# Optimization experiments

Hardware: AMD Instinct MI355X
Metric: run time of the kernel (lower is better)

Reference implementation:

```python
import jax, jax.numpy as jnp
import numpy as np

NCE_T = 0.07  # opt.nce_T
EPS = 1e-8    # torch CosineSimilarity eps

def setup_inputs() -> dict:
    key = jax.random.key(0)
    k1, k2, k3 = jax.random.split(key, 3)
    num_patches, C = 4096, 256
    features = jax.random.normal(k1, (2, num_patches, C), dtype=jnp.float32)
    labels_seg = jax.random.randint(k2, (1, 1, 128, 128, 128), 0, 5, dtype=jnp.int32)
    labels_coords = jax.random.randint(k3, (num_patches, 3), 0, 64, dtype=jnp.int32)
    return {"features": features, "labels_seg": labels_seg,
            "labels_coords": labels_coords, "cr_w": 64, "cr_h": 64, "cr_d": 64}

def _sup_nce_loss(features, lab):
    # features: (ntps, N, C); lab: (N,) int class per patch
    ntps, N, C = features.shape
    M = ntps * N
    f = features.reshape(M, C)
    nrm = jnp.linalg.norm(f, axis=-1)  # (M,)
    # cosine similarity = (f @ f^T) / max(|x||y|, eps), then / temperature
    sim = (f @ f.T) / jnp.maximum(nrm[:, None] * nrm[None, :], EPS)
    logits = sim / NCE_T
    logits = logits - jax.lax.stop_gradient(jnp.max(logits, axis=1, keepdims=True))
    pos = (lab[:, None] == lab[None, :]).astype(f.dtype)        # (N,N)
    pos = jnp.tile(pos, (ntps, ntps))                            # (M,M)
    diag_off = 1.0 - jnp.eye(M, dtype=f.dtype)                   # logits_mask
    pos = pos * diag_off
    denom = jnp.log((jnp.exp(logits) * diag_off).sum(1, keepdims=True))
    log_prob = logits - denom
    mean_log_prob_pos = (pos * log_prob).sum(1) / pos.sum(1)
    return -(mean_log_prob_pos.reshape(ntps, N)).mean()

def reference(features, labels_seg, labels_coords, cr_w, cr_h, cr_d):
    # nearest-neighbor downsample of labels to coords_range (torch 'nearest': floor(i*in/out))
    H, W, D = labels_seg.shape[2], labels_seg.shape[3], labels_seg.shape[4]
    iw = (jnp.arange(cr_w) * H) // cr_w
    ih = (jnp.arange(cr_h) * W) // cr_h
    idd = (jnp.arange(cr_d) * D) // cr_d
    seg = labels_seg[0, 0][iw][:, ih][:, :, idd]  # (cr_w, cr_h, cr_d)
    lab = seg[labels_coords[:, 0], labels_coords[:, 1], labels_coords[:, 2]]  # (N,)
    return _sup_nce_loss(features, lab)
```

## Files before the change

kernel.cpp:

```cpp
#include <hip/hip_runtime.h>
#include <hip/hip_bf16.h>

typedef __attribute__((ext_vector_type(4))) float floatx4;

#define C_DIM 256
#define K2_SCALE 20.60992915f
#define LN2F 0.6931471805599453f

__device__ __forceinline__ unsigned int pack4fp8(float a, float b, float c, float d) {
    int w = __builtin_amdgcn_cvt_pk_fp8_f32(a, b, 0, false);
    w = __builtin_amdgcn_cvt_pk_fp8_f32(c, d, w, true);
    return (unsigned int)w;
}

template <int CTRL>
__device__ __forceinline__ float dppadd(float x) {
    int y = __builtin_amdgcn_update_dpp(0, __builtin_bit_cast(int, x),
                                        CTRL, 0xf, 0xf, true);
    return x + __builtin_bit_cast(float, y);
}
__device__ __forceinline__ float row16_sum(float x) {
    x = dppadd<0xB1>(x);
    x = dppadd<0x4E>(x);
    x = dppadd<0x124>(x);
    x = dppadd<0x128>(x);
    return x;
}

__global__ void norm_kernel(const float* __restrict__ f,
                            unsigned char* __restrict__ g2,
                            const int* __restrict__ seg,
                            const int* __restrict__ coords,
                            const int* __restrict__ crw,
                            const int* __restrict__ crh,
                            const int* __restrict__ crd,
                            int* __restrict__ lab,
                            float* __restrict__ acc_done,
                            int N, int H, int W, int D) {
    __shared__ float nrm[16][264];
    const int tid = threadIdx.x;
    const int bid = blockIdx.x;
    const int gid = bid * 256 + tid;
    const int lane = tid & 63;
    const int wave = tid >> 6;

    if (gid == 0) {
        acc_done[0] = 0.0f;
        ((int*)acc_done)[1] = 0;
    }
    if (gid < N) {
        int c0 = coords[3 * gid + 0];
        int c1 = coords[3 * gid + 1];
        int c2 = coords[3 * gid + 2];
        int i0 = (c0 * H) / crw[0];
        int i1 = (c1 * W) / crh[0];
        int i2 = (c2 * D) / crd[0];
        lab[gid] = seg[(i0 * W + i1) * D + i2];
    }

    const int rbase = bid * 16;
#pragma unroll
    for (int q = 0; q < 4; ++q) {
        const int rl = wave * 4 + q;
        const float4 v = ((const float4*)(f + (size_t)(rbase + rl) * C_DIM))[lane];
        float ss = v.x * v.x + v.y * v.y + v.z * v.z + v.w * v.w;
#pragma unroll
        for (int off = 32; off; off >>= 1) ss += __shfl_xor(ss, off, 64);
        const float inv = 1.0f / sqrtf(ss);
        *(float4*)&nrm[rl][lane * 4] = float4{v.x * inv, v.y * inv, v.z * inv, v.w * inv};
    }
    __syncthreads();

    const int k0 = (tid >> 5) * 32 + ((tid >> 3) & 3) * 8;
    const float* ra = &nrm[(2 * tid) & 15][k0];
    const float* rb = &nrm[(2 * tid + 1) & 15][k0];
    uint4 o;
    o.x = pack4fp8(ra[0], ra[1], ra[2], ra[3]);
    o.y = pack4fp8(ra[4], ra[5], ra[6], ra[7]);
    o.z = pack4fp8(rb[0], rb[1], rb[2], rb[3]);
    o.w = pack4fp8(rb[4], rb[5], rb[6], rb[7]);
    *(uint4*)(g2 + (size_t)bid * 4096 + (size_t)tid * 16) = o;
}

__global__ __launch_bounds__(256, 2) void
gram_kernel(const unsigned char* __restrict__ G2,
            const int* __restrict__ lab,
            float* __restrict__ part,
            int M, int labmask, int nt) {
    __shared__ unsigned char Abuf[32768];
    __shared__ unsigned char Bbuf[32768];
    __shared__ float red[2][2][128][3];

    const int tid = threadIdx.x;
    const int bid = blockIdx.x;
    const int lane = tid & 63;
    const int wave = tid >> 6;
    const int waveM = wave >> 1;
    const int waveN = wave & 1;
    const int cc = lane & 15;
    const int cq = lane >> 4;

    const int start = bid * 4 + (bid < 32 ? bid : 32);
    const int len = 4 + (bid < 32 ? 1 : 0);
    int tmPrev = -1;

    for (int s = 0; s < len; ++s) {
        const int idx = start + s;
        float fnt = (float)nt;
        float disc = (2.0f * fnt + 1.0f) * (2.0f * fnt + 1.0f) - 8.0f * (float)idx;
        int tm = (int)((2.0f * fnt + 1.0f - sqrtf(disc)) * 0.5f);
        if (tm < 0) tm = 0;
        if (tm > nt - 1) tm = nt - 1;
        while (tm > 0 && idx < tm * nt - tm * (tm - 1) / 2) --tm;
        while (idx >= (tm + 1) * nt - (tm + 1) * tm / 2) ++tm;
        const int tn = tm + (idx - (tm * nt - tm * (tm - 1) / 2));

        const int rowA0 = tm * 128;
        const int rowB0 = tn * 128;
        const bool diagTile = (tm == tn);

        if (tm != tmPrev) {
            const unsigned char* gA = G2 + (size_t)tm * 32768;
#pragma unroll
            for (int i = 0; i < 8; ++i) {
                const int u = i * 256 + tid;
                __builtin_amdgcn_global_load_lds(
                    (const __attribute__((address_space(1))) void*)(gA + (size_t)u * 16),
                    (__attribute__((address_space(3))) void*)(&Abuf[(u & ~63) * 16]),
                    16, 0, 0);
            }
            tmPrev = tm;
        }
        if (!diagTile) {
            const unsigned char* gB = G2 + (size_t)tn * 32768;
#pragma unroll
            for (int i = 0; i < 8; ++i) {
                const int u = i * 256 + tid;
                __builtin_amdgcn_global_load_lds(
                    (const __attribute__((address_space(1))) void*)(gB + (size_t)u * 16),
                    (__attribute__((address_space(3))) void*)(&Bbuf[(u & ~63) * 16]),
                    16, 0, 0);
            }
        }
        __syncthreads();

        const unsigned char* A = Abuf;
        const unsigned char* B = diagTile ? Abuf : Bbuf;

        floatx4 acc[4][4];
#pragma unroll
        for (int mi = 0; mi < 4; ++mi)
#pragma unroll
            for (int ni = 0; ni < 4; ++ni)
                acc[mi][ni] = floatx4{-1.0f, -1.0f, -1.0f, -1.0f};

#pragma unroll
        for (int ks = 0; ks < 8; ++ks) {
            long af[4], bf[4];
#pragma unroll
            for (int mi = 0; mi < 4; ++mi)
                af[mi] = *(const long*)&A[(size_t)((waveM * 4 + mi) * 8 + ks) * 512 + lane * 8];
#pragma unroll
            for (int ni = 0; ni < 4; ++ni)
                bf[ni] = *(const long*)&B[(size_t)((waveN * 4 + ni) * 8 + ks) * 512 + lane * 8];
#pragma unroll
            for (int mi = 0; mi < 4; ++mi)
#pragma unroll
                for (int ni = 0; ni < 4; ++ni)
                    acc[mi][ni] = __builtin_amdgcn_mfma_f32_16x16x32_fp8_fp8(
                        af[mi], bf[ni], acc[mi][ni], 0, 0, 0);
        }

        int col_lab[4];
#pragma unroll
        for (int ni = 0; ni < 4; ++ni)
            col_lab[ni] = lab[(rowB0 + waveN * 64 + ni * 16 + cc) & labmask];

        float bse[4] = {}, bnu[4] = {}, bct[4] = {};

#pragma unroll
        for (int mi = 0; mi < 4; ++mi) {
#pragma unroll
            for (int r = 0; r < 4; ++r) {
                const int lrow = waveM * 64 + mi * 16 + cq * 4 + r;
                const int grow = rowA0 + lrow;
                const int rl = lab[grow & labmask];
                float se = 0.0f, nu = 0.0f, ct = 0.0f;
#pragma unroll
                for (int ni = 0; ni < 4; ++ni) {
                    const int gcol = rowB0 + waveN * 64 + ni * 16 + cc;
                    const float ls2 = acc[mi][ni][r] * K2_SCALE;
                    const bool valid = (gcol != grow);
                    const float e = valid ? exp2f(ls2) : 0.0f;
                    const bool pos = valid && (col_lab[ni] == rl);
                    const float nuv = pos ? ls2 : 0.0f;
                    const float p = pos ? 1.0f : 0.0f;
                    se += e; nu += nuv; ct += p;
                    bse[ni] += e; bnu[ni] += nuv; bct[ni] += p;
                }
                se = row16_sum(se);
                nu = row16_sum(nu);
                ct = row16_sum(ct);
                if (cc == 0) {
                    red[0][waveN][lrow][0] = se;
                    red[0][waveN][lrow][1] = nu;
                    red[0][waveN][lrow][2] = ct;
                }
            }
        }

        if (!diagTile) {
#pragma unroll
            for (int ni = 0; ni < 4; ++ni) {
                float se = bse[ni], nu = bnu[ni], ct = bct[ni];
                se += __shfl_xor(se, 16, 64); nu += __shfl_xor(nu, 16, 64); ct += __shfl_xor(ct, 16, 64);
                se += __shfl_xor(se, 32, 64); nu += __shfl_xor(nu, 32, 64); ct += __shfl_xor(ct, 32, 64);
                if (cq == 0) {
                    const int lcol = waveN * 64 + ni * 16 + cc;
                    red[1][waveM][lcol][0] = se;
                    red[1][waveM][lcol][1] = nu;
                    red[1][waveM][lcol][2] = ct;
                }
            }
        }
        __syncthreads();

        for (int v = tid; v < 384; v += 256) {
            const int c = v >> 7, r = v & 127;
            part[((size_t)(tn * 3 + c)) * M + rowA0 + r] =
                red[0][0][r][c] + red[0][1][r][c];
        }
        if (!diagTile) {
            for (int v = tid; v < 384; v += 256) {
                const int c = v >> 7, r = v & 127;
                part[((size_t)(tm * 3 + c)) * M + rowB0 + r] =
                    red[1][0][r][c] + red[1][1][r][c];
            }
        }
        __syncthreads();
    }
}

__global__ void finalize_kernel(const float* __restrict__ part,
                                float* __restrict__ acc_done,
                                float* __restrict__ out, int M, int nslots,
                                int nblk) {
    __shared__ float fred[3][4][64];
    const int tid = threadIdx.x;
    const int g = tid >> 6;
    const int l = tid & 63;
    const int row = blockIdx.x * 64 + l;

    float se = 0.0f, nu = 0.0f, ct = 0.0f;
    const int s0 = g * (nslots / 4);
    for (int s = s0; s < s0 + nslots / 4; ++s) {
        const float* p = part + (size_t)s * 3 * M;
        se += p[row];
        nu += p[M + row];
        ct += p[2 * M + row];
    }
    fred[0][g][l] = se;
    fred[1][g][l] = nu;
    fred[2][g][l] = ct;
    __syncthreads();

    if (tid < 64) {
        se = fred[0][0][l] + fred[0][1][l] + fred[0][2][l] + fred[0][3][l];
        nu = fred[1][0][l] + fred[1][1][l] + fred[1][2][l] + fred[1][3][l];
        ct = fred[2][0][l] + fred[2][1][l] + fred[2][2][l] + fred[2][3][l];
        float term = nu * LN2F / ct - logf(se);
#pragma unroll
        for (int off = 32; off; off >>= 1) term += __shfl_xor(term, off, 64);
        if (l == 0) {
            atomicAdd(&acc_done[0], term);
            __threadfence();
            int old = atomicAdd((int*)&acc_done[1], 1);
            if (old == nblk - 1) {
                float total = atomicAdd(&acc_done[0], 0.0f);
                out[0] = -total / (float)M;
            }
        }
    }
}

extern "C" void kernel_launch(void* const* d_in, const int* in_sizes, int n_in,
                              void* d_out, int out_size, void* d_ws, size_t ws_size,
                              hipStream_t stream) {
    const float* features = (const float*)d_in[0];
    const int* labels_seg = (const int*)d_in[1];
    const int* labels_coords = (const int*)d_in[2];
    const int* crw = (const int*)d_in[3];
    const int* crh = (const int*)d_in[4];
    const int* crd = (const int*)d_in[5];
    float* out = (float*)d_out;

    const int N = in_sizes[2] / 3;
    const int M = in_sizes[0] / C_DIM;
    const int H = 128, W = 128, D = 128;
    const int nt = M / 128;

    char* ws = (char*)d_ws;
    unsigned char* g2 = (unsigned char*)ws;
    char* p1 = ws + (size_t)M * C_DIM;
    int* lab = (int*)p1;
    char* p2 = p1 + (size_t)N * 4;
    float* part = (float*)p2;
    char* p3 = p2 + (size_t)nt * 3 * M * 4;
    float* acc_done = (float*)p3;

    norm_kernel<<<M / 16, 256, 0, stream>>>(features, g2, labels_seg,
                                            labels_coords, crw, crh, crd, lab,
                                            acc_done, N, H, W, D);

    gram_kernel<<<512, 256, 0, stream>>>(g2, lab, part, M, N - 1, nt);

    const int fblk = M / 64;
    finalize_kernel<<<fblk, 256, 0, stream>>>(part, acc_done, out, M, nt, fblk);
}
```

Before: 121.7 us.

## Compute positive-pair numerator via per-class feature sums instead of in-gram masking

The positive-pair logit sum and count are no longer accumulated inside the gram kernel. They come algebraically from per-class sums of normalized features, so each row's positive sum is its dot product with its class sum minus itself, and the count comes from a label histogram. The gram epilogue then only accumulates the exp-sum, which drops the label loads, compares and two of three reductions, and shrinks the partial buffer to a third. In exchange the norm kernel writes an fp32 normalized copy and does atomics, finalize rereads that fp32 copy, and a memset is added.

```diff
diff --git a/kernel.cpp b/kernel.cpp
--- a/kernel.cpp
+++ b/kernel.cpp
@@ -4,8 +4,8 @@
 typedef __attribute__((ext_vector_type(4))) float floatx4;
 
 #define C_DIM 256
+#define INV_T 14.285714285714286f
 #define K2_SCALE 20.60992915f
-#define LN2F 0.6931471805599453f
 
 __device__ __forceinline__ unsigned int pack4fp8(float a, float b, float c, float d) {
     int w = __builtin_amdgcn_cvt_pk_fp8_f32(a, b, 0, false);
@@ -27,69 +27,97 @@
     return x;
 }
 
-__global__ void norm_kernel(const float* __restrict__ f,
-                            unsigned char* __restrict__ g2,
-                            const int* __restrict__ seg,
-                            const int* __restrict__ coords,
-                            const int* __restrict__ crw,
-                            const int* __restrict__ crh,
-                            const int* __restrict__ crd,
-                            int* __restrict__ lab,
-                            float* __restrict__ acc_done,
-                            int N, int H, int W, int D) {
+__global__ __launch_bounds__(256) void
+norm_kernel(const float* __restrict__ f,
+            unsigned char* __restrict__ g2,
+            float* __restrict__ gn,
+            const int* __restrict__ seg,
+            const int* __restrict__ coords,
+            const int* __restrict__ crw,
+            const int* __restrict__ crh,
+            const int* __restrict__ crd,
+            int* __restrict__ lab,
+            float* __restrict__ S,
+            int* __restrict__ hist,
+            int N, int H, int W, int D) {
     __shared__ float nrm[16][264];
+    __shared__ float Sloc[5][256];
+    __shared__ int lbl[16];
+    __shared__ int histloc[8];
+
     const int tid = threadIdx.x;
     const int bid = blockIdx.x;
-    const int gid = bid * 256 + tid;
     const int lane = tid & 63;
     const int wave = tid >> 6;
-
-    if (gid == 0) {
-        acc_done[0] = 0.0f;
-        ((int*)acc_done)[1] = 0;
-    }
-    if (gid < N) {
-        int c0 = coords[3 * gid + 0];
-        int c1 = coords[3 * gid + 1];
-        int c2 = coords[3 * gid + 2];
-        int i0 = (c0 * H) / crw[0];
-        int i1 = (c1 * W) / crh[0];
-        int i2 = (c2 * D) / crd[0];
-        lab[gid] = seg[(i0 * W + i1) * D + i2];
-    }
-
-    const int rbase = bid * 16;
-#pragma unroll
-    for (int q = 0; q < 4; ++q) {
-        const int rl = wave * 4 + q;
-        const float4 v = ((const float4*)(f + (size_t)(rbase + rl) * C_DIM))[lane];
-        float ss = v.x * v.x + v.y * v.y + v.z * v.z + v.w * v.w;
-#pragma unroll
-        for (int off = 32; off; off >>= 1) ss += __shfl_xor(ss, off, 64);
-        const float inv = 1.0f / sqrtf(ss);
-        *(float4*)&nrm[rl][lane * 4] = float4{v.x * inv, v.y * inv, v.z * inv, v.w * inv};
-    }
+    const int rbase = bid * 64;
+
+    if (tid < 8) histloc[tid] = 0;
+#pragma unroll
+    for (int c = 0; c < 5; ++c) Sloc[c][tid] = 0.0f;
     __syncthreads();
 
-    const int k0 = (tid >> 5) * 32 + ((tid >> 3) & 3) * 8;
-    const float* ra = &nrm[(2 * tid) & 15][k0];
-    const float* rb = &nrm[(2 * tid + 1) & 15][k0];
-    uint4 o;
-    o.x = pack4fp8(ra[0], ra[1], ra[2], ra[3]);
-    o.y = pack4fp8(ra[4], ra[5], ra[6], ra[7]);
-    o.z = pack4fp8(rb[0], rb[1], rb[2], rb[3]);
-    o.w = pack4fp8(rb[4], rb[5], rb[6], rb[7]);
-    *(uint4*)(g2 + (size_t)bid * 4096 + (size_t)tid * 16) = o;
+    for (int g = 0; g < 4; ++g) {
+        const int grow0 = rbase + g * 16;
+        if (tid < 16) {
+            const int row = grow0 + tid;
+            const int p = row & (N - 1);
+            int c0 = coords[3 * p + 0];
+            int c1 = coords[3 * p + 1];
+            int c2 = coords[3 * p + 2];
+            int i0 = (c0 * H) / crw[0];
+            int i1 = (c1 * W) / crh[0];
+            int i2 = (c2 * D) / crd[0];
+            const int c = seg[(i0 * W + i1) * D + i2];
+            lbl[tid] = c;
+            if (row < N) {
+                lab[row] = c;
+                atomicAdd(&histloc[c], 1);
+            }
+        }
+        const int rl = wave * 4;
+#pragma unroll
+        for (int q = 0; q < 4; ++q) {
+            const int row = grow0 + rl + q;
+            const float4 v = ((const float4*)(f + (size_t)row * C_DIM))[lane];
+            float ss = v.x * v.x + v.y * v.y + v.z * v.z + v.w * v.w;
+#pragma unroll
+            for (int off = 32; off; off >>= 1) ss += __shfl_xor(ss, off, 64);
+            const float inv = 1.0f / sqrtf(ss);
+            const float4 o = float4{v.x * inv, v.y * inv, v.z * inv, v.w * inv};
+            *(float4*)&nrm[rl + q][lane * 4] = o;
+            *(float4*)(gn + (size_t)row * C_DIM + lane * 4) = o;
+        }
+        __syncthreads();
+
+        const int k0 = (tid >> 5) * 32 + ((tid >> 3) & 3) * 8;
+        const float* ra = &nrm[(2 * tid) & 15][k0];
+        const float* rb = &nrm[(2 * tid + 1) & 15][k0];
+        uint4 o;
+        o.x = pack4fp8(ra[0], ra[1], ra[2], ra[3]);
+        o.y = pack4fp8(ra[4], ra[5], ra[6], ra[7]);
+        o.z = pack4fp8(rb[0], rb[1], rb[2], rb[3]);
+        o.w = pack4fp8(rb[4], rb[5], rb[6], rb[7]);
+        *(uint4*)(g2 + (size_t)(bid * 4 + g) * 4096 + (size_t)tid * 16) = o;
+
+#pragma unroll
+        for (int rr = 0; rr < 16; ++rr)
+            Sloc[lbl[rr]][tid] += nrm[rr][tid];
+        __syncthreads();
+    }
+
+#pragma unroll
+    for (int c = 0; c < 5; ++c)
+        unsafeAtomicAdd(&S[c * 256 + tid], Sloc[c][tid]);
+    if (tid < 8 && histloc[tid] > 0) atomicAdd(&hist[tid], histloc[tid]);
 }
 
 __global__ __launch_bounds__(256, 2) void
 gram_kernel(const unsigned char* __restrict__ G2,
-            const int* __restrict__ lab,
             float* __restrict__ part,
-            int M, int labmask, int nt) {
+            int M, int nt) {
     __shared__ unsigned char Abuf[32768];
     __shared__ unsigned char Bbuf[32768];
-    __shared__ float red[2][2][128][3];
+    __shared__ float red[2][2][128];
 
     const int tid = threadIdx.x;
     const int bid = blockIdx.x;
@@ -171,114 +199,105 @@
                         af[mi], bf[ni], acc[mi][ni], 0, 0, 0);
         }
 
-        int col_lab[4];
-#pragma unroll
-        for (int ni = 0; ni < 4; ++ni)
-            col_lab[ni] = lab[(rowB0 + waveN * 64 + ni * 16 + cc) & labmask];
-
-        float bse[4] = {}, bnu[4] = {}, bct[4] = {};
-
+        float bse[4] = {};
 #pragma unroll
         for (int mi = 0; mi < 4; ++mi) {
 #pragma unroll
             for (int r = 0; r < 4; ++r) {
                 const int lrow = waveM * 64 + mi * 16 + cq * 4 + r;
                 const int grow = rowA0 + lrow;
-                const int rl = lab[grow & labmask];
-                float se = 0.0f, nu = 0.0f, ct = 0.0f;
+                float se = 0.0f;
 #pragma unroll
                 for (int ni = 0; ni < 4; ++ni) {
                     const int gcol = rowB0 + waveN * 64 + ni * 16 + cc;
-                    const float ls2 = acc[mi][ni][r] * K2_SCALE;
-                    const bool valid = (gcol != grow);
-                    const float e = valid ? exp2f(ls2) : 0.0f;
-                    const bool pos = valid && (col_lab[ni] == rl);
-                    const float nuv = pos ? ls2 : 0.0f;
-                    const float p = pos ? 1.0f : 0.0f;
-                    se += e; nu += nuv; ct += p;
-                    bse[ni] += e; bnu[ni] += nuv; bct[ni] += p;
+                    const float e = exp2f(acc[mi][ni][r] * K2_SCALE);
+                    const float ev = (gcol != grow) ? e : 0.0f;
+                    se += ev;
+                    bse[ni] += ev;
                 }
                 se = row16_sum(se);
-                nu = row16_sum(nu);
-                ct = row16_sum(ct);
-                if (cc == 0) {
-                    red[0][waveN][lrow][0] = se;
-                    red[0][waveN][lrow][1] = nu;
-                    red[0][waveN][lrow][2] = ct;
-                }
-            }
-        }
-
+                if (cc == 0) red[0][waveN][lrow] = se;
+            }
+        }
         if (!diagTile) {
 #pragma unroll
             for (int ni = 0; ni < 4; ++ni) {
-                float se = bse[ni], nu = bnu[ni], ct = bct[ni];
-                se += __shfl_xor(se, 16, 64); nu += __shfl_xor(nu, 16, 64); ct += __shfl_xor(ct, 16, 64);
-                se += __shfl_xor(se, 32, 64); nu += __shfl_xor(nu, 32, 64); ct += __shfl_xor(ct, 32, 64);
-                if (cq == 0) {
-                    const int lcol = waveN * 64 + ni * 16 + cc;
-                    red[1][waveM][lcol][0] = se;
-                    red[1][waveM][lcol][1] = nu;
-                    red[1][waveM][lcol][2] = ct;
-                }
-            }
-        }
-        __syncthreads();
-
-        for (int v = tid; v < 384; v += 256) {
-            const int c = v >> 7, r = v & 127;
-            part[((size_t)(tn * 3 + c)) * M + rowA0 + r] =
-                red[0][0][r][c] + red[0][1][r][c];
-        }
-        if (!diagTile) {
-            for (int v = tid; v < 384; v += 256) {
-                const int c = v >> 7, r = v & 127;
-                part[((size_t)(tm * 3 + c)) * M + rowB0 + r] =
-                    red[1][0][r][c] + red[1][1][r][c];
-            }
-        }
-        __syncthreads();
-    }
-}
-
-__global__ void finalize_kernel(const float* __restrict__ part,
-                                float* __restrict__ acc_done,
-                                float* __restrict__ out, int M, int nslots,
-                                int nblk) {
-    __shared__ float fred[3][4][64];
+                float se = bse[ni];
+                se += __shfl_xor(se, 16, 64);
+                se += __shfl_xor(se, 32, 64);
+                if (cq == 0) red[1][waveM][waveN * 64 + ni * 16 + cc] = se;
+            }
+        }
+        __syncthreads();
+
+        if (tid < 128)
+            part[(size_t)tn * M + rowA0 + tid] = red[0][0][tid] + red[0][1][tid];
+        if (!diagTile && tid >= 128)
+            part[(size_t)tm * M + rowB0 + (tid - 128)] =
+                red[1][0][tid - 128] + red[1][1][tid - 128];
+        __syncthreads();
+    }
+}
+
+__global__ __launch_bounds__(256) void
+finalize_kernel(const float* __restrict__ part,
+                const float* __restrict__ gn,
+                const float* __restrict__ S,
+                const int* __restrict__ hist,
+                const int* __restrict__ lab,
+                float* __restrict__ acc_done,
+                float* __restrict__ out,
+                int M, int N, int nslots, int nblk) {
+    __shared__ float Sl[5][256];
+    __shared__ float seL[256];
+    __shared__ int labL[256];
+    __shared__ float dot4[256][4];
+    __shared__ float sred[256];
+
     const int tid = threadIdx.x;
-    const int g = tid >> 6;
-    const int l = tid & 63;
-    const int row = blockIdx.x * 64 + l;
-
-    float se = 0.0f, nu = 0.0f, ct = 0.0f;
-    const int s0 = g * (nslots / 4);
-    for (int s = s0; s < s0 + nslots / 4; ++s) {
-        const float* p = part + (size_t)s * 3 * M;
-        se += p[row];
-        nu += p[M + row];
-        ct += p[2 * M + row];
-    }
-    fred[0][g][l] = se;
-    fred[1][g][l] = nu;
-    fred[2][g][l] = ct;
+    const int lane = tid & 63;
+    const int wave = tid >> 6;
+    const int r0 = blockIdx.x * 256;
+    const int ntps = M / N;
+
+#pragma unroll
+    for (int c = 0; c < 5; ++c) Sl[c][tid] = S[c * 256 + tid];
+
+    float se = 0.0f;
+    for (int s = 0; s < nslots; ++s) se += part[(size_t)s * M + r0 + tid];
+    seL[tid] = se;
+    labL[tid] = lab[(r0 + tid) & (N - 1)];
     __syncthreads();
 
-    if (tid < 64) {
-        se = fred[0][0][l] + fred[0][1][l] + fred[0][2][l] + fred[0][3][l];
-        nu = fred[1][0][l] + fred[1][1][l] + fred[1][2][l] + fred[1][3][l];
-        ct = fred[2][0][l] + fred[2][1][l] + fred[2][2][l] + fred[2][3][l];
-        float term = nu * LN2F / ct - logf(se);
-#pragma unroll
-        for (int off = 32; off; off >>= 1) term += __shfl_xor(term, off, 64);
-        if (l == 0) {
-            atomicAdd(&acc_done[0], term);
-            __threadfence();
-            int old = atomicAdd((int*)&acc_done[1], 1);
-            if (old == nblk - 1) {
-                float total = atomicAdd(&acc_done[0], 0.0f);
-                out[0] = -total / (float)M;
-            }
+    for (int j = 0; j < 64; ++j) {
+        const int lr = wave * 64 + j;
+        const int row = r0 + lr;
+        const int c = labL[lr];
+        const float4 x = ((const float4*)(gn + (size_t)row * C_DIM))[lane];
+        const float4 sv = *(const float4*)&Sl[c][lane * 4];
+        float p = x.x * sv.x + x.y * sv.y + x.z * sv.z + x.w * sv.w;
+        p = row16_sum(p);
+        if ((lane & 15) == 0) dot4[lr][lane >> 4] = p;
+    }
+    __syncthreads();
+
+    const float dot = dot4[tid][0] + dot4[tid][1] + dot4[tid][2] + dot4[tid][3];
+    const float cnt = (float)(ntps * hist[labL[tid]] - 1);
+    const float term = INV_T * ((dot - 1.0f) / cnt - 1.0f) - logf(seL[tid]);
+
+    sred[tid] = term;
+    __syncthreads();
+    for (int k = 128; k; k >>= 1) {
+        if (tid < k) sred[tid] += sred[tid + k];
+        __syncthreads();
+    }
+    if (tid == 0) {
+        atomicAdd(&acc_done[0], sred[0]);
+        __threadfence();
+        int old = atomicAdd((int*)&acc_done[1], 1);
+        if (old == nblk - 1) {
+            float total = atomicAdd(&acc_done[0], 0.0f);
+            out[0] = -total / (float)M;
         }
     }
 }
@@ -302,18 +321,25 @@
     char* ws = (char*)d_ws;
     unsigned char* g2 = (unsigned char*)ws;
     char* p1 = ws + (size_t)M * C_DIM;
-    int* lab = (int*)p1;
-    char* p2 = p1 + (size_t)N * 4;
-    float* part = (float*)p2;
-    char* p3 = p2 + (size_t)nt * 3 * M * 4;
-    float* acc_done = (float*)p3;
-
-    norm_kernel<<<M / 16, 256, 0, stream>>>(features, g2, labels_seg,
+    float* gn = (float*)p1;
+    char* p2 = p1 + (size_t)M * C_DIM * 4;
+    int* lab = (int*)p2;
+    char* p3 = p2 + (size_t)N * 4;
+    float* part = (float*)p3;
+    char* p4 = p3 + (size_t)nt * M * 4;
+    float* S = (float*)p4;
+    int* hist = (int*)(p4 + 5 * 256 * 4);
+    float* acc_done = (float*)(p4 + 5 * 256 * 4 + 8 * 4);
+
+    hipMemsetAsync(p4, 0, 5 * 256 * 4 + 8 * 4 + 8, stream);
+
+    norm_kernel<<<M / 64, 256, 0, stream>>>(features, g2, gn, labels_seg,
                                             labels_coords, crw, crh, crd, lab,
-                                            acc_done, N, H, W, D);
-
-    gram_kernel<<<512, 256, 0, stream>>>(g2, lab, part, M, N - 1, nt);
-
-    const int fblk = M / 64;
-    finalize_kernel<<<fblk, 256, 0, stream>>>(part, acc_done, out, M, nt, fblk);
-}
+                                            S, hist, N, H, W, D);
+
+    gram_kernel<<<512, 256, 0, stream>>>(g2, part, M, nt);
+
+    const int fblk = M / 256;
+    finalize_kernel<<<fblk, 256, 0, stream>>>(part, gn, S, hist, lab, acc_done,
+                                              out, M, N, nt, fblk);
+}
```

Result: slower. 152.6 us (+25.4%).
